# Kernel optimization log

Measured on AMD Instinct MI355X. Metric: run time of the kernel, lower is better.

Reference implementation:

```python
import jax, jax.numpy as jnp
import numpy as np

P = 4          # num_perturbations
N = 50000      # nodes
E = 800000     # edges
IN = 64        # input_dim == hidden_dim (allows stacked conv weights)
H = 64         # args.hidden_dim
OUT = 10       # output_dim (classes)
G = 512        # num graphs in batch
DROP_P = 0.1   # node-drop prob p
EPS = 1e-5     # BatchNorm eps


def setup_inputs() -> dict:
    key = jax.random.key(0)
    ks = jax.random.split(key, 8)
    x = jax.random.normal(ks[0], (N, IN), jnp.float32)
    edge_index = jax.random.randint(ks[1], (2, E), 0, N, dtype=jnp.int64)
    batch = jnp.sort(jax.random.randint(ks[2], (N,), 0, G, dtype=jnp.int64))
    drop_mask = jax.random.bernoulli(ks[3], DROP_P, (P, N))
    conv_w = jax.random.normal(ks[4], (4, H, H), jnp.float32) * (1.0 / np.sqrt(H))
    conv_b = jnp.zeros((4, H), jnp.float32)
    bn_gamma = jnp.ones((4, H), jnp.float32)
    bn_beta = jnp.zeros((4, H), jnp.float32)
    fc_w = jax.random.normal(ks[5], (5, H, OUT), jnp.float32) * (1.0 / np.sqrt(H))
    fc_b = jnp.zeros((5, OUT), jnp.float32)
    return {"x": x, "edge_index": edge_index, "batch": batch, "drop_mask": drop_mask,
            "conv_w": conv_w, "conv_b": conv_b, "bn_gamma": bn_gamma,
            "bn_beta": bn_beta, "fc_w": fc_w, "fc_b": fc_b}


def reference(x, edge_index, batch, drop_mask, conv_w, conv_b, bn_gamma, bn_beta, fc_w, fc_b):
    P_, N_ = drop_mask.shape
    n_tot = P_ * N_
    # node dropping per perturbation: x -> [P, N, F] with dropped rows zeroed
    x_rep = jnp.where(drop_mask[:, :, None], jnp.zeros((), x.dtype), x[None, :, :])
    # replicate edge_index across perturbations with offset (max+1), as in torch code
    offset = jnp.max(edge_index) + 1
    shift = offset * jnp.arange(P_, dtype=edge_index.dtype)[:, None]
    src = (edge_index[0][None, :] + shift).reshape(-1)
    dst = (edge_index[1][None, :] + shift).reshape(-1)
    # GCN symmetric normalization with self-loops (PyG GCNConv default)
    deg = jax.ops.segment_sum(jnp.ones(src.shape, jnp.float32), dst, num_segments=n_tot) + 1.0
    dinv = jax.lax.rsqrt(deg)
    norm_e = dinv[src] * dinv[dst]        # edge messages
    norm_s = dinv * dinv                   # self-loop messages

    h = x_rep.reshape(n_tot, -1)
    outs = [x_rep]
    for i in range(4):
        hw = h @ conv_w[i]                 # [n_tot, H]
        agg = jax.ops.segment_sum(norm_e[:, None] * hw[src], dst, num_segments=n_tot)
        h = agg + norm_s[:, None] * hw + conv_b[i]
        # BatchNorm1d (training mode: batch stats, biased variance)
        mu = h.mean(axis=0)
        var = h.var(axis=0)
        h = (h - mu) * jax.lax.rsqrt(var + EPS) * bn_gamma[i] + bn_beta[i]
        h = jax.nn.relu(h)
        outs.append(h.reshape(P_, N_, -1))

    out = None
    for i, o in enumerate(outs):
        pooled = jax.ops.segment_sum(o.mean(axis=0), batch, num_segments=G)  # global_add_pool
        y = pooled @ fc_w[i] + fc_b[i]     # dropout skipped (eval)
        out = y if out is None else out + y
    return jax.nn.log_softmax(out, axis=-1)
```

## Files before the change

kernel.cpp:

```cpp
#include <hip/hip_runtime.h>

#define N_NODES 50000
#define N_EDGES 800000
#define P_PERT  4
#define NTOT    (P_PERT * N_NODES)
#define HDIM    64
#define NGRAPH  512
#define NCLASS  10
#define BN_EPS  1e-5f
#define SCAN_BLOCKS ((N_NODES + 255) / 256)
#define BN_SLICES 64
#define SAH_STRIDE 72
#define SC_STRIDE 72
#define ZERO_FLOATS 297120
#define PSTRIDE ((size_t)(N_NODES + 1) * 32)
#define GATHER_BLOCKS (((N_NODES + 63) / 64) * 8)

typedef _Float16 half4 __attribute__((ext_vector_type(4)));
typedef _Float16 f16x8 __attribute__((ext_vector_type(8)));
typedef float    f32x4 __attribute__((ext_vector_type(4)));
typedef unsigned short u16x8 __attribute__((ext_vector_type(8)));



__global__ void count_kernel(const int* __restrict__ ei, int* __restrict__ cnt,
                             int* __restrict__ slot) {
    int j = blockIdx.x * blockDim.x + threadIdx.x;
    if (j >= N_EDGES) return;
    slot[j] = atomicAdd(&cnt[ei[N_EDGES + j]], 1);
}

__global__ void scan_reduce(const int* __restrict__ cnt, int* __restrict__ bsum,
                            float* __restrict__ dinv) {
    __shared__ int sdata[256];
    int i = blockIdx.x * 256 + threadIdx.x;
    int v = (i < N_NODES) ? cnt[i] : 0;
    if (i < N_NODES) dinv[i] = rsqrtf((float)v + 1.0f);
    sdata[threadIdx.x] = (v + 7) & ~7;
    __syncthreads();
    for (int off = 128; off > 0; off >>= 1) {
        if (threadIdx.x < off) sdata[threadIdx.x] += sdata[threadIdx.x + off];
        __syncthreads();
    }
    if (threadIdx.x == 0) bsum[blockIdx.x] = sdata[0];
}

__global__ void scan_tops(const int* __restrict__ bsum, int* __restrict__ boff,
                          int* __restrict__ rowptr) {
    __shared__ int sdata[256];
    int t = threadIdx.x;
    int v = (t < SCAN_BLOCKS) ? bsum[t] : 0;
    sdata[t] = v;
    __syncthreads();
    for (int off = 1; off < 256; off <<= 1) {
        int tmp = (t >= off) ? sdata[t - off] : 0;
        __syncthreads();
        sdata[t] += tmp;
        __syncthreads();
    }
    if (t < SCAN_BLOCKS) boff[t] = sdata[t] - v;
    if (t == 255) rowptr[N_NODES] = sdata[255];
}

__global__ void scan_write(const int* __restrict__ cnt, const int* __restrict__ boff,
                           int* __restrict__ rowptr) {
    __shared__ int sdata[256];
    int i = blockIdx.x * 256 + threadIdx.x;
    int v = (i < N_NODES) ? ((cnt[i] + 7) & ~7) : 0;
    sdata[threadIdx.x] = v;
    __syncthreads();
    for (int off = 1; off < 256; off <<= 1) {
        int tmp = (threadIdx.x >= off) ? sdata[threadIdx.x - off] : 0;
        __syncthreads();
        sdata[threadIdx.x] += tmp;
        __syncthreads();
    }
    if (i < N_NODES) rowptr[i] = boff[blockIdx.x] + sdata[threadIdx.x] - v;
}

__global__ void fill_kernel(const int* __restrict__ ei, const int* __restrict__ rowptr,
                            const int* __restrict__ slot, unsigned short* __restrict__ csr) {
    int j = blockIdx.x * blockDim.x + threadIdx.x;
    if (j >= N_EDGES) return;
    int s = ei[j], d = ei[N_EDGES + j];
    csr[rowptr[d] + slot[j]] = (unsigned short)s;
}

__global__ void pad_kernel(const int* __restrict__ cnt, const int* __restrict__ rowptr,
                           unsigned short* __restrict__ csr) {
    int v = blockIdx.x * 256 + threadIdx.x;
    if (v >= N_NODES) return;
    int c = cnt[v], cp = (c + 7) & ~7, base = rowptr[v];
    for (int j = c; j < cp; ++j) csr[base + j] = (unsigned short)N_NODES;
}

__global__ void wpack_zero_kernel(const float* __restrict__ W, _Float16* __restrict__ wpack,
                                  float* __restrict__ zreg, _Float16* __restrict__ hwh2) {
    int idx = blockIdx.x * 256 + threadIdx.x;
    if (idx < 4 * 4096) {
        int e = idx & 4095;
        int j = e & 7;
        int lane = (e >> 3) & 63;
        int ntkh = e >> 9;
        int kh = ntkh >> 2, nt = ntkh & 3;
        int m = lane & 15, quad = lane >> 4;
        wpack[idx] = (_Float16)W[(idx >> 12) * 4096 + (kh * 32 + quad * 8 + j) * 64 + nt * 16 + m];
    }
    if (idx < 256) {
        hwh2[(size_t)(idx >> 5) * PSTRIDE + (size_t)N_NODES * 32 + (idx & 31)] = (_Float16)0.0f;
    }
    for (int i = idx; i < ZERO_FLOATS; i += gridDim.x * 256) zreg[i] = 0.0f;
}

__global__ void bn_reduce(const float* __restrict__ bn, const float* __restrict__ gamma,
                          const float* __restrict__ beta, float* __restrict__ bnss) {
    __shared__ float part[4][128];
    __shared__ float tot[128];
    int t = threadIdx.x;
    int f = t & 127, q = t >> 7;
    float s = 0.0f;
#pragma unroll
    for (int i = 0; i < 16; ++i) s += bn[(q * 16 + i) * 128 + f];
    part[q][f] = s;
    __syncthreads();
    if (t < 128) tot[t] = part[0][t] + part[1][t] + part[2][t] + part[3][t];
    __syncthreads();
    if (t < 64) {
        float su = tot[t], sq = tot[64 + t];
        const float inv_n = 1.0f / (float)NTOT;
        float mu = su * inv_n;
        float var = sq * inv_n - mu * mu;
        float sc = gamma[t] * rsqrtf(var + BN_EPS);
        bnss[t] = sc;
        bnss[64 + t] = beta[t] - mu * sc;
    }
}

template <int LAYER0>
__global__ __launch_bounds__(256) void gemm_fused(const void* __restrict__ srcv,
        const int* __restrict__ mask, const float* __restrict__ bnss,
        const int* __restrict__ batch, const _Float16* __restrict__ wpack,
        const float* __restrict__ dinv, _Float16* __restrict__ hwh,
        float* __restrict__ pooled) {
    __shared__ _Float16 sAh[64 * SAH_STRIDE];
    __shared__ _Float16 sC[64 * SC_STRIDE];
    int tid = threadIdx.x;
    size_t rowbase = (size_t)blockIdx.x * 64;
    int lane = tid & 63;
    int wv = tid >> 6;
    int bg[16];
#pragma unroll
    for (int rr = 0; rr < 16; ++rr)
        bg[rr] = batch[(int)((rowbase + wv * 16 + rr) % N_NODES)];
    const f16x8* wp = (const f16x8*)wpack;
    f16x8 bfrag[2][4];
#pragma unroll
    for (int kh = 0; kh < 2; ++kh)
#pragma unroll
        for (int nt = 0; nt < 4; ++nt)
            bfrag[kh][nt] = wp[(kh * 4 + nt) * 64 + lane];
    int r0 = tid >> 4;
    int f4l = (tid & 15) * 4;
    float4 sc4, sh4;
    if (!LAYER0) {
        sc4 = *(const float4*)&bnss[f4l];
        sh4 = *(const float4*)&bnss[64 + f4l];
    }
#pragma unroll
    for (int it = 0; it < 4; ++it) {
        int r = r0 + it * 16;
        int grow = (int)rowbase + r;
        float4 val;
        if (LAYER0) {
            const float* src = (const float*)srcv;
            int p = grow / N_NODES, v = grow - p * N_NODES;
            if (mask[p * N_NODES + v]) {
                val = make_float4(0.f, 0.f, 0.f, 0.f);
            } else {
                val = *(const float4*)&src[(size_t)v * HDIM + f4l];
            }
        } else {
            const _Float16* src = (const _Float16*)srcv;
            half4 hv = *(const half4*)&src[(size_t)grow * HDIM + f4l];
            val.x = fmaxf((float)hv.x * sc4.x + sh4.x, 0.0f);
            val.y = fmaxf((float)hv.y * sc4.y + sh4.y, 0.0f);
            val.z = fmaxf((float)hv.z * sc4.z + sh4.z, 0.0f);
            val.w = fmaxf((float)hv.w * sc4.w + sh4.w, 0.0f);
        }
        half4 hv4 = {(_Float16)val.x, (_Float16)val.y, (_Float16)val.z, (_Float16)val.w};
        *(half4*)&sAh[r * SAH_STRIDE + f4l] = hv4;
    }
    __syncthreads();
    int m = lane & 15;
    int quad = lane >> 4;
    f32x4 acc4[4];
#pragma unroll
    for (int nt = 0; nt < 4; ++nt) acc4[nt] = (f32x4){0.f, 0.f, 0.f, 0.f};
#pragma unroll
    for (int kh = 0; kh < 2; ++kh) {
        f16x8 a = *(const f16x8*)&sAh[(wv * 16 + m) * SAH_STRIDE + kh * 32 + quad * 8];
#pragma unroll
        for (int nt = 0; nt < 4; ++nt)
            acc4[nt] = __builtin_amdgcn_mfma_f32_16x16x32_f16(a, bfrag[kh][nt], acc4[nt], 0, 0, 0);
    }
#pragma unroll
    for (int reg = 0; reg < 4; ++reg) {
        int crow = wv * 16 + quad * 4 + reg;
        int growc = (int)rowbase + crow;
        int vc = growc % N_NODES;
        float dsc = dinv[vc];
#pragma unroll
        for (int nt = 0; nt < 4; ++nt)
            sC[crow * SC_STRIDE + nt * 16 + m] = (_Float16)(acc4[nt][reg] * dsc);
    }
    __syncthreads();
    {
        int r = tid >> 2, c = tid & 3;
        int grow = (int)rowbase + r;
        int p = grow / N_NODES, v = grow - p * N_NODES;
        _Float16* dst0 = &hwh[(size_t)(p * 2 + 0) * PSTRIDE + (size_t)v * 32];
        _Float16* dst1 = &hwh[(size_t)(p * 2 + 1) * PSTRIDE + (size_t)v * 32];
        *(f16x8*)&dst0[c * 8] = *(f16x8*)&sC[r * SC_STRIDE + c * 8];
        *(f16x8*)&dst1[c * 8] = *(f16x8*)&sC[r * SC_STRIDE + (c + 4) * 8];
    }
    {
        int f = lane;
        int curg = -1;
        float acc = 0.0f;
#pragma unroll
        for (int rr = 0; rr < 16; ++rr) {
            int g = bg[rr];
            if (g != curg) {
                if (curg >= 0) atomicAdd(&pooled[curg * HDIM + f], acc * (1.0f / P_PERT));
                curg = g;
                acc = 0.0f;
            }
            acc += (float)sAh[(wv * 16 + rr) * SAH_STRIDE + f];
        }
        atomicAdd(&pooled[curg * HDIM + f], acc * (1.0f / P_PERT));
    }
}

__global__ __launch_bounds__(256) void gather_bn(const _Float16* __restrict__ hwh2,
        const int* __restrict__ rowptr, const unsigned short* __restrict__ csr,
        const float* __restrict__ dinv, const float* __restrict__ b,
        _Float16* __restrict__ h, float* __restrict__ bn) {
    __shared__ float lsum[4][4][8];
    __shared__ float lssq[4][4][8];
    int tid = threadIdx.x;
    int lane = tid & 63;
    int wv = tid >> 6;
    int part = blockIdx.x & 7;
    int grp = blockIdx.x >> 3;
    int p = part >> 1, fh = part & 1;
    int n16 = lane >> 2;
    int f16 = lane & 3;
    int v = grp * 64 + wv * 16 + n16;
    bool valid = v < N_NODES;
    int vv = valid ? v : N_NODES;
    int kb = 0, ke = 0;
    float di = 0.0f;
    if (valid) { kb = rowptr[v]; ke = rowptr[v + 1]; di = dinv[v]; }
    const _Float16* lsrc = hwh2 + (size_t)part * PSTRIDE + f16 * 8;
    f16x8 sv = *(const f16x8*)&lsrc[(size_t)vv * 32];
    float acc[8];
#pragma unroll
    for (int j = 0; j < 8; ++j) acc[j] = 0.0f;
    u16x8 ci = {};
    if (kb < ke) ci = *(const u16x8*)&csr[kb];
    for (int k = kb; k < ke; k += 8) {
        u16x8 cin = {};
        if (k + 8 < ke) cin = *(const u16x8*)&csr[k + 8];
        f16x8 m0 = *(const f16x8*)&lsrc[(size_t)ci[0] * 32];
        f16x8 m1 = *(const f16x8*)&lsrc[(size_t)ci[1] * 32];
        f16x8 m2 = *(const f16x8*)&lsrc[(size_t)ci[2] * 32];
        f16x8 m3 = *(const f16x8*)&lsrc[(size_t)ci[3] * 32];
        f16x8 m4 = *(const f16x8*)&lsrc[(size_t)ci[4] * 32];
        f16x8 m5 = *(const f16x8*)&lsrc[(size_t)ci[5] * 32];
        f16x8 m6 = *(const f16x8*)&lsrc[(size_t)ci[6] * 32];
        f16x8 m7 = *(const f16x8*)&lsrc[(size_t)ci[7] * 32];
        f16x8 s = ((m0 + m1) + (m2 + m3)) + ((m4 + m5) + (m6 + m7));
#pragma unroll
        for (int j = 0; j < 8; ++j) acc[j] += (float)s[j];
        ci = cin;
    }
    float hv[8], qv[8];
    float4 b0 = *(const float4*)&b[fh * 32 + f16 * 8];
    float4 b1 = *(const float4*)&b[fh * 32 + f16 * 8 + 4];
    float bb[8] = {b0.x, b0.y, b0.z, b0.w, b1.x, b1.y, b1.z, b1.w};
#pragma unroll
    for (int j = 0; j < 8; ++j) {
        float x = valid ? fmaf(di, acc[j] + (float)sv[j], bb[j]) : 0.0f;
        hv[j] = x;
        qv[j] = x * x;
    }
    if (valid) {
        f16x8 hh;
#pragma unroll
        for (int j = 0; j < 8; ++j) hh[j] = (_Float16)hv[j];
        __builtin_nontemporal_store(hh,
            (f16x8*)&h[((size_t)p * N_NODES + (size_t)v) * HDIM + fh * 32 + f16 * 8]);
    }
#pragma unroll
    for (int d = 4; d <= 32; d <<= 1) {
#pragma unroll
        for (int j = 0; j < 8; ++j) {
            hv[j] += __shfl_xor(hv[j], d);
            qv[j] += __shfl_xor(qv[j], d);
        }
    }
    if (lane < 4) {
#pragma unroll
        for (int j = 0; j < 8; ++j) {
            lsum[wv][f16][j] = hv[j];
            lssq[wv][f16][j] = qv[j];
        }
    }
    __syncthreads();
    if (tid < 32) {
        int q = tid >> 3, j = tid & 7;
        float s = lsum[0][q][j] + lsum[1][q][j] + lsum[2][q][j] + lsum[3][q][j];
        float qq = lssq[0][q][j] + lssq[1][q][j] + lssq[2][q][j] + lssq[3][q][j];
        float* bns = bn + (blockIdx.x & (BN_SLICES - 1)) * 128;
        int f = fh * 32 + q * 8 + j;
        atomicAdd(&bns[f], s);
        atomicAdd(&bns[64 + f], qq);
    }
}

__global__ void final_pool(const _Float16* __restrict__ h, const float* __restrict__ bnss,
                           const int* __restrict__ batch, float* __restrict__ pooled) {
    int f = threadIdx.x & 63;
    int sg = threadIdx.x >> 6;
    int vb = blockIdx.x * 16 + sg * 4;
    float sc = bnss[f], sh = bnss[64 + f];
    int curg = -1;
    float acc = 0.0f;
#pragma unroll
    for (int i = 0; i < 4; ++i) {
        int v = vb + i;
        if (v >= N_NODES) break;
        float s = 0.0f;
#pragma unroll
        for (int p = 0; p < P_PERT; ++p) {
            size_t idx = ((size_t)(p * N_NODES + v)) * HDIM + f;
            s += fmaxf((float)h[idx] * sc + sh, 0.0f);
        }
        int g = batch[v];
        if (g != curg) {
            if (curg >= 0) atomicAdd(&pooled[curg * HDIM + f], acc * (1.0f / P_PERT));
            curg = g;
            acc = 0.0f;
        }
        acc += s;
    }
    if (curg >= 0) atomicAdd(&pooled[curg * HDIM + f], acc * (1.0f / P_PERT));
}

__global__ void head_kernel(const float* __restrict__ pooled, const float* __restrict__ fcw,
                            const float* __restrict__ fcb, float* __restrict__ out) {
    int g = blockIdx.x;
    __shared__ float y[NCLASS];
    __shared__ float lse;
    int c = threadIdx.x;
    if (c < NCLASS) {
        float acc = 0.0f;
        for (int i = 0; i < 5; ++i) {
            acc += fcb[i * NCLASS + c];
            const float* pr = &pooled[((size_t)i * NGRAPH + g) * HDIM];
            const float* w = &fcw[i * HDIM * NCLASS + c];
            for (int k = 0; k < HDIM; ++k) acc += pr[k] * w[k * NCLASS];
        }
        y[c] = acc;
    }
    __syncthreads();
    if (threadIdx.x == 0) {
        float m = y[0];
        for (int i = 1; i < NCLASS; ++i) m = fmaxf(m, y[i]);
        float s = 0.0f;
        for (int i = 0; i < NCLASS; ++i) s += expf(y[i] - m);
        lse = m + logf(s);
    }
    __syncthreads();
    if (c < NCLASS) out[g * NCLASS + c] = y[c] - lse;
}

extern "C" void kernel_launch(void* const* d_in, const int* in_sizes, int n_in,
                              void* d_out, int out_size, void* d_ws, size_t ws_size,
                              hipStream_t stream) {
    const float* x      = (const float*)d_in[0];
    const int*   ei     = (const int*)d_in[1];
    const int*   batch  = (const int*)d_in[2];
    const int*   mask   = (const int*)d_in[3];
    const float* conv_w = (const float*)d_in[4];
    const float* conv_b = (const float*)d_in[5];
    const float* gamma  = (const float*)d_in[6];
    const float* beta   = (const float*)d_in[7];
    const float* fcw    = (const float*)d_in[8];
    const float* fcb    = (const float*)d_in[9];
    float* out = (float*)d_out;

    char* ws = (char*)d_ws;
    int*      cnt     = (int*)(ws + 0);
    float*    pooled  = (float*)(ws + 400000);
    float*    bn      = (float*)(ws + 1055360);
    float*    bnss    = (float*)(ws + 1186432);
    int*      rowptr  = (int*)(ws + 1188480);
    float*    dinv    = (float*)(ws + 1388484);
    unsigned short* csr = (unsigned short*)(ws + 1588496);
    _Float16* h       = (_Float16*)(ws + 3989504);
    _Float16* hwh     = (_Float16*)(ws + 29589504);
    int*      bsum    = (int*)(ws + 55190016);
    int*      boff    = (int*)(ws + 55191040);
    _Float16* wpack   = (_Float16*)(ws + 55192064);
    int*      slot    = (int*)(ws + 55224832);

    wpack_zero_kernel<<<512, 256, 0, stream>>>(conv_w, wpack, (float*)ws, hwh);
    count_kernel<<<(N_EDGES + 255) / 256, 256, 0, stream>>>(ei, cnt, slot);
    scan_reduce<<<SCAN_BLOCKS, 256, 0, stream>>>(cnt, bsum, dinv);
    scan_tops<<<1, 256, 0, stream>>>(bsum, boff, rowptr);
    scan_write<<<SCAN_BLOCKS, 256, 0, stream>>>(cnt, boff, rowptr);
    fill_kernel<<<(N_EDGES + 255) / 256, 256, 0, stream>>>(ei, rowptr, slot, csr);
    pad_kernel<<<SCAN_BLOCKS, 256, 0, stream>>>(cnt, rowptr, csr);

    for (int i = 0; i < 4; ++i) {
        float* bni = bn + i * BN_SLICES * 128;
        if (i == 0)
            gemm_fused<1><<<NTOT / 64, 256, 0, stream>>>(x, mask, nullptr,
                                                         batch, wpack, dinv, hwh, pooled);
        else
            gemm_fused<0><<<NTOT / 64, 256, 0, stream>>>(h, nullptr, bnss + (i - 1) * 128,
                                                         batch, wpack + (size_t)i * 4096,
                                                         dinv, hwh,
                                                         pooled + (size_t)i * NGRAPH * HDIM);
        gather_bn<<<GATHER_BLOCKS, 256, 0, stream>>>(hwh, rowptr, csr, dinv,
                                                     conv_b + i * HDIM, h, bni);
        bn_reduce<<<1, 512, 0, stream>>>(bni, gamma + i * HDIM, beta + i * HDIM,
                                         bnss + i * 128);
    }
    final_pool<<<(N_NODES + 15) / 16, 256, 0, stream>>>(
        h, bnss + 3 * 128, batch, pooled + (size_t)4 * NGRAPH * HDIM);
    head_kernel<<<NGRAPH, 64, 0, stream>>>(pooled, fcw, fcb, out);
}
```

Before: 399.1 us.

## Sort nodes into degree buckets so gather wavefronts process similar-degree rows

Adds a three-kernel bucket sort that groups nodes by padded in-degree (in units of 8) and builds a permutation array. gather_bn now processes nodes in that permuted order, so the lanes of a wavefront run loops of similar length and spend less time idle while one lane finishes a long row. The cost is three extra small kernels, one more indirection load per node, and a loss of spatial locality in the self-row reads and output writes. The BN partial sums stay correct because they are order-independent.

```diff
diff --git a/kernel.cpp b/kernel.cpp
--- a/kernel.cpp
+++ b/kernel.cpp
@@ -10,6 +10,7 @@
 #define BN_EPS  1e-5f
 #define SCAN_BLOCKS ((N_NODES + 255) / 256)
 #define BN_SLICES 64
+#define NBUCKET 64
 #define SAH_STRIDE 72
 #define SC_STRIDE 72
 #define ZERO_FLOATS 297120
@@ -92,6 +93,33 @@
     if (v >= N_NODES) return;
     int c = cnt[v], cp = (c + 7) & ~7, base = rowptr[v];
     for (int j = c; j < cp; ++j) csr[base + j] = (unsigned short)N_NODES;
+}
+
+__global__ void bucket_hist(const int* __restrict__ cnt, int* __restrict__ bcnt) {
+    int v = blockIdx.x * 256 + threadIdx.x;
+    if (v >= N_NODES) return;
+    int b = min((cnt[v] + 7) >> 3, NBUCKET - 1);
+    atomicAdd(&bcnt[b], 1);
+}
+
+__global__ void bucket_scan(const int* __restrict__ bcnt, int* __restrict__ boff2) {
+    int t = threadIdx.x;
+    int raw = bcnt[t];
+    int v = raw;
+    for (int d = 1; d < 64; d <<= 1) {
+        int u = __shfl_up(v, d);
+        if (t >= d) v += u;
+    }
+    boff2[t] = v - raw;
+}
+
+__global__ void bucket_scatter(const int* __restrict__ cnt, const int* __restrict__ boff2,
+                               int* __restrict__ bcur, int* __restrict__ perm) {
+    int v = blockIdx.x * 256 + threadIdx.x;
+    if (v >= N_NODES) return;
+    int b = min((cnt[v] + 7) >> 3, NBUCKET - 1);
+    int pos = boff2[b] + atomicAdd(&bcur[b], 1);
+    perm[pos] = v;
 }
 
 __global__ void wpack_zero_kernel(const float* __restrict__ W, _Float16* __restrict__ wpack,
@@ -244,6 +272,7 @@
 __global__ __launch_bounds__(256) void gather_bn(const _Float16* __restrict__ hwh2,
         const int* __restrict__ rowptr, const unsigned short* __restrict__ csr,
         const float* __restrict__ dinv, const float* __restrict__ b,
+        const int* __restrict__ perm,
         _Float16* __restrict__ h, float* __restrict__ bn) {
     __shared__ float lsum[4][4][8];
     __shared__ float lssq[4][4][8];
@@ -255,14 +284,14 @@
     int p = part >> 1, fh = part & 1;
     int n16 = lane >> 2;
     int f16 = lane & 3;
-    int v = grp * 64 + wv * 16 + n16;
-    bool valid = v < N_NODES;
-    int vv = valid ? v : N_NODES;
+    int slotv = grp * 64 + wv * 16 + n16;
+    bool valid = slotv < N_NODES;
+    int vp = valid ? perm[slotv] : N_NODES;
     int kb = 0, ke = 0;
     float di = 0.0f;
-    if (valid) { kb = rowptr[v]; ke = rowptr[v + 1]; di = dinv[v]; }
+    if (valid) { kb = rowptr[vp]; ke = rowptr[vp + 1]; di = dinv[vp]; }
     const _Float16* lsrc = hwh2 + (size_t)part * PSTRIDE + f16 * 8;
-    f16x8 sv = *(const f16x8*)&lsrc[(size_t)vv * 32];
+    f16x8 sv = *(const f16x8*)&lsrc[(size_t)vp * 32];
     float acc[8];
 #pragma unroll
     for (int j = 0; j < 8; ++j) acc[j] = 0.0f;
@@ -299,7 +328,7 @@
 #pragma unroll
         for (int j = 0; j < 8; ++j) hh[j] = (_Float16)hv[j];
         __builtin_nontemporal_store(hh,
-            (f16x8*)&h[((size_t)p * N_NODES + (size_t)v) * HDIM + fh * 32 + f16 * 8]);
+            (f16x8*)&h[((size_t)p * N_NODES + (size_t)vp) * HDIM + fh * 32 + f16 * 8]);
     }
 #pragma unroll
     for (int d = 4; d <= 32; d <<= 1) {
@@ -402,6 +431,9 @@
 
     char* ws = (char*)d_ws;
     int*      cnt     = (int*)(ws + 0);
+    int*      bcnt    = (int*)(ws + 200000);
+    int*      bcur    = (int*)(ws + 200256);
+    int*      boff2   = (int*)(ws + 200512);
     float*    pooled  = (float*)(ws + 400000);
     float*    bn      = (float*)(ws + 1055360);
     float*    bnss    = (float*)(ws + 1186432);
@@ -414,12 +446,16 @@
     int*      boff    = (int*)(ws + 55191040);
     _Float16* wpack   = (_Float16*)(ws + 55192064);
     int*      slot    = (int*)(ws + 55224832);
+    int*      perm    = (int*)(ws + 58424832);
 
     wpack_zero_kernel<<<512, 256, 0, stream>>>(conv_w, wpack, (float*)ws, hwh);
     count_kernel<<<(N_EDGES + 255) / 256, 256, 0, stream>>>(ei, cnt, slot);
+    bucket_hist<<<SCAN_BLOCKS, 256, 0, stream>>>(cnt, bcnt);
     scan_reduce<<<SCAN_BLOCKS, 256, 0, stream>>>(cnt, bsum, dinv);
     scan_tops<<<1, 256, 0, stream>>>(bsum, boff, rowptr);
     scan_write<<<SCAN_BLOCKS, 256, 0, stream>>>(cnt, boff, rowptr);
+    bucket_scan<<<1, 64, 0, stream>>>(bcnt, boff2);
+    bucket_scatter<<<SCAN_BLOCKS, 256, 0, stream>>>(cnt, boff2, bcur, perm);
     fill_kernel<<<(N_EDGES + 255) / 256, 256, 0, stream>>>(ei, rowptr, slot, csr);
     pad_kernel<<<SCAN_BLOCKS, 256, 0, stream>>>(cnt, rowptr, csr);
 
@@ -434,7 +470,7 @@
                                                          dinv, hwh,
                                                          pooled + (size_t)i * NGRAPH * HDIM);
         gather_bn<<<GATHER_BLOCKS, 256, 0, stream>>>(hwh, rowptr, csr, dinv,
-                                                     conv_b + i * HDIM, h, bni);
+                                                     conv_b + i * HDIM, perm, h, bni);
         bn_reduce<<<1, 512, 0, stream>>>(bni, gamma + i * HDIM, beta + i * HDIM,
                                          bnss + i * 128);
     }
```

Result: slower. 1.180 ms (+195.6%).
